# Performance work log

Measured on AMD Instinct MI355X. Metric: run time of the kernel, lower is better.

The kernel has to match this reference:

```python
import jax, jax.numpy as jnp
import numpy as np

N, E, DIN, DOUT, NNZ = 8192, 4096, 256, 128, 65536
TEMP = float(DOUT) ** 0.5
NEG = -1e9


def setup_inputs() -> dict:
    key = jax.random.key(0)
    ks = jax.random.split(key, 8)
    stdv = 1.0 / np.sqrt(DOUT)
    u = lambda k, shp: jax.random.uniform(k, shp, jnp.float32, -stdv, stdv)
    x = jax.random.normal(ks[0], (N, DIN), jnp.float32)
    nodes = jax.random.randint(ks[1], (NNZ,), 0, N, jnp.int32)
    edges = jax.random.randint(ks[2], (NNZ,), 0, E, jnp.int32)
    hyperedge_index = jnp.stack([nodes, edges])  # [2, nnz]
    return {
        "x": x,
        "weight": u(ks[3], (DIN, DOUT)),   # transfer weight
        "weight2": u(ks[4], (DIN, DOUT)),
        "weight3": u(ks[5], (DOUT, DOUT)),
        "bias": u(ks[6], (DOUT,)),
        "q_ctx": u(ks[7], (DOUT,)),        # word_context.weight[0]
        "hyperedge_index": hyperedge_index,
        "num_nodes": N,
        "num_edges": E,
    }


def reference(x, weight, weight2, weight3, bias, q_ctx, hyperedge_index, num_nodes, num_edges):
    # dense incidence H[node, edge] = 1  (hyperedge_preprocess)
    H = jnp.zeros((num_nodes, num_edges), x.dtype).at[
        hyperedge_index[0], hyperedge_index[1]].set(1.0)
    adj = H.T                       # [E, N]  (mask / original attention for attn1)

    x4 = x @ weight2                # [N, D]  x_4att
    xt = x @ weight + bias          # [N, D]  transferred features (v of attn1)

    # ---- attention1: query = shared word-context vector, keys = x4 ----
    row = (q_ctx / TEMP) @ x4.T                    # [N] (q1 rows are identical)
    scores1 = jnp.where(adj == 0, NEG, row[None, :])  # [E, N]
    att1 = jax.nn.softmax(adj, axis=-1) + jax.nn.softmax(scores1, axis=-1)
    edge = att1 @ xt                               # [E, D]

    att2he = att1.T                                # [N, E]

    # ---- attention2: queries = x4, keys = edge @ W3 ----
    edge4 = edge @ weight3                         # [E, D]
    scores2 = jnp.where(adj.T == 0, NEG, (x4 / TEMP) @ edge4.T)  # [N, E]
    att2hn = jax.nn.softmax(adj.T, axis=-1) + jax.nn.softmax(scores2, axis=-1)

    # ---- fused outer-product attention and output projection ----
    A = att2he @ att2he.T + att2hn @ att2hn.T      # [N, N]
    h_prime_g = jax.nn.elu(A @ x4)                 # [N, D]
    return h_prime_g
```

## Files before the change

kernel.cpp:

```cpp
#include <hip/hip_runtime.h>
#include <math.h>

constexpr int Nn   = 8192;
constexpr int Ee   = 4096;
constexpr int DIN  = 256;
constexpr int DOUT = 128;
constexpr int NNZ  = 65536;
constexpr int EC   = 96;
constexpr int NC   = 48;

#define TEMPR 0.08838834764831845f
#define EM1   1.7182818284590452f

typedef __attribute__((ext_vector_type(8))) short short8;
typedef __attribute__((ext_vector_type(4))) float f32x4;

static __device__ __forceinline__ float wave_sum64(float v) {
#pragma unroll
    for (int m = 32; m; m >>= 1) v += __shfl_xor(v, m, 64);
    return v;
}
static __device__ __forceinline__ float wave_max64(float v) {
#pragma unroll
    for (int m = 32; m; m >>= 1) v = fmaxf(v, __shfl_xor(v, m, 64));
    return v;
}
static __device__ __forceinline__ short f2bf(float f) {
    union { float f; unsigned u; } v; v.f = f;
    const unsigned r = (v.u + 0x7FFFu + ((v.u >> 16) & 1u)) >> 16;
    return (short)r;
}
static __device__ __forceinline__ unsigned packbf2(float a, float b) {
    return ((unsigned)(unsigned short)f2bf(a)) |
           (((unsigned)(unsigned short)f2bf(b)) << 16);
}
static __device__ __forceinline__ float2 unpackbf2(unsigned u) {
    union { unsigned u; float f; } lo, hi;
    lo.u = u << 16; hi.u = u & 0xFFFF0000u;
    return make_float2(lo.f, hi.f);
}

__global__ __launch_bounds__(256) void k_ww3(
    const float* __restrict__ W, const float* __restrict__ W2,
    const float* __restrict__ W3, const float* __restrict__ bias,
    short* __restrict__ W2T, short* __restrict__ WWT, float* __restrict__ bW3)
{
    const int b = blockIdx.x;
    const int t = threadIdx.x;
    if (b < 32) {
        __shared__ float sW[8][128];
        const int r0 = b * 8;
        for (int i = t; i < 1024; i += 256)
            sW[i >> 7][i & 127] = W[(size_t)(r0 + (i >> 7)) * DOUT + (i & 127)];
        __syncthreads();
        const int c  = t & 127;
        const int rh = (t >> 7) * 4;
        float acc[4] = {0.f, 0.f, 0.f, 0.f};
        for (int k = 0; k < 128; ++k) {
            const float w3 = W3[(size_t)k * DOUT + c];
#pragma unroll
            for (int i = 0; i < 4; ++i) acc[i] = fmaf(sW[rh + i][k], w3, acc[i]);
        }
#pragma unroll
        for (int i = 0; i < 4; ++i)
            WWT[(size_t)c * DIN + (r0 + rh + i)] = f2bf(acc[i]);
    } else if (b < 40) {
        const int k0 = (b - 32) * 32;
        for (int i = t; i < 32 * 128; i += 256) {
            const int k = k0 + (i >> 7);
            const int n = i & 127;
            W2T[(size_t)n * DIN + k] = f2bf(W2[(size_t)k * DOUT + n]);
        }
    } else {
        if (t < 128) {
            float acc = 0.f;
            for (int k = 0; k < 128; ++k)
                acc = fmaf(bias[k], W3[(size_t)k * DOUT + t], acc);
            bW3[t] = acc;
        }
    }
}

__global__ __launch_bounds__(256) void k_gemm1f(
    const float* __restrict__ x, const short* __restrict__ W2T,
    const short* __restrict__ WWT, const float* __restrict__ bW3,
    const float* __restrict__ q, const int* __restrict__ hidx,
    unsigned* __restrict__ bitmap, int* __restrict__ degE, int* __restrict__ degN,
    int* __restrict__ csrEn, int* __restrict__ csrNe, int* __restrict__ csrNs,
    short* __restrict__ x4b, short* __restrict__ xwb,
    float* __restrict__ rowv, float* __restrict__ csx4, float* __restrict__ csxw)
{
    __shared__ float s4[DOUT], sw[DOUT], srow[16];
    const int t    = threadIdx.x;
    const int lane = t & 63;
    const int wv   = t >> 6;
    const int n16  = lane & 15;
    const int quad = lane >> 4;
    const int r0   = blockIdx.x * 16;
    const int n0   = wv * 32;

    const unsigned gid = blockIdx.x * 256 + t;
    if (gid < NNZ) {
        const int n = hidx[gid];
        const int e = hidx[NNZ + gid];
        const unsigned word = (unsigned)n * (unsigned)Ee + (unsigned)e;
        const unsigned bit  = 1u << (word & 31u);
        const unsigned old  = atomicOr(&bitmap[word >> 5], bit);
        if (!(old & bit)) {
            const int pe = atomicAdd(&degE[e], 1);
            if (pe < EC) {
                csrEn[e * EC + pe] = n;
                const int pn = atomicAdd(&degN[n], 1);
                if (pn < NC) {
                    csrNe[n * NC + pn] = e;
                    csrNs[n * NC + pn] = e * EC + pe;
                }
            }
        }
    }

    f32x4 acc4[2], accw[2];
#pragma unroll
    for (int nt = 0; nt < 2; ++nt) {
        acc4[nt] = (f32x4){0.f, 0.f, 0.f, 0.f};
        accw[nt] = (f32x4){0.f, 0.f, 0.f, 0.f};
    }
#pragma unroll
    for (int k0 = 0; k0 < DIN; k0 += 32) {
        const int kb = k0 + quad * 8;
        const float4 xa = *(const float4*)&x[(size_t)(r0 + n16) * DIN + kb];
        const float4 xb = *(const float4*)&x[(size_t)(r0 + n16) * DIN + kb + 4];
        short8 af;
        af[0] = f2bf(xa.x); af[1] = f2bf(xa.y); af[2] = f2bf(xa.z); af[3] = f2bf(xa.w);
        af[4] = f2bf(xb.x); af[5] = f2bf(xb.y); af[6] = f2bf(xb.z); af[7] = f2bf(xb.w);
#pragma unroll
        for (int nt = 0; nt < 2; ++nt) {
            const int col = n0 + nt * 16 + n16;
            const short8 b4 = *(const short8*)&W2T[(size_t)col * DIN + kb];
            const short8 bw = *(const short8*)&WWT[(size_t)col * DIN + kb];
            acc4[nt] = __builtin_amdgcn_mfma_f32_16x16x32_bf16(af, b4, acc4[nt], 0, 0, 0);
            accw[nt] = __builtin_amdgcn_mfma_f32_16x16x32_bf16(af, bw, accw[nt], 0, 0, 0);
        }
    }

    float bwv[2], qv[2];
#pragma unroll
    for (int nt = 0; nt < 2; ++nt) {
        const int col = n0 + nt * 16 + n16;
        bwv[nt] = bW3[col];
        qv[nt]  = q[col];
    }
#pragma unroll
    for (int nt = 0; nt < 2; ++nt) {
        const int col = n0 + nt * 16 + n16;
#pragma unroll
        for (int reg = 0; reg < 4; ++reg) {
            const int row = r0 + quad * 4 + reg;
            x4b[(size_t)row * DOUT + col] = f2bf(acc4[nt][reg]);
            xwb[(size_t)row * DOUT + col] = f2bf(accw[nt][reg] + bwv[nt]);
        }
    }
    float pr[4];
#pragma unroll
    for (int reg = 0; reg < 4; ++reg)
        pr[reg] = qv[0] * acc4[0][reg] + qv[1] * acc4[1][reg];
#pragma unroll
    for (int m = 8; m; m >>= 1) {
#pragma unroll
        for (int reg = 0; reg < 4; ++reg) pr[reg] += __shfl_xor(pr[reg], m, 64);
    }
    if (t < 16) srow[t] = 0.f;
    if (t < DOUT) { s4[t] = 0.f; sw[t] = 0.f; }
    __syncthreads();
    if (n16 == 0) {
#pragma unroll
        for (int reg = 0; reg < 4; ++reg) atomicAdd(&srow[quad * 4 + reg], pr[reg]);
    }
#pragma unroll
    for (int nt = 0; nt < 2; ++nt) {
        const int col = n0 + nt * 16 + n16;
        const float c4s = acc4[nt][0] + acc4[nt][1] + acc4[nt][2] + acc4[nt][3];
        const float cws = accw[nt][0] + accw[nt][1] + accw[nt][2] + accw[nt][3]
                        + 4.f * bwv[nt];
        atomicAdd(&s4[col], c4s);
        atomicAdd(&sw[col], cws);
    }
    __syncthreads();
    if (t < 16) rowv[r0 + t] = srow[t] * TEMPR;
    if (t < DOUT) { atomicAdd(&csx4[t], s4[t]); atomicAdd(&csxw[t], sw[t]); }
}

__global__ __launch_bounds__(256) void k_edge1(
    const int* __restrict__ degE, const int* __restrict__ csrEn,
    const float* __restrict__ rowv,
    const float* __restrict__ csx4, const float* __restrict__ csxw,
    const unsigned* __restrict__ x4b, const unsigned* __restrict__ xwb,
    float* __restrict__ Sval, unsigned* __restrict__ e4b, unsigned* __restrict__ G1b,
    float* __restrict__ wsArr, float* __restrict__ c2g)
{
    __shared__ int   sN[4][EC];
    __shared__ float sS[4][EC];
    __shared__ float sC2[4];
    const int t    = threadIdx.x;
    const int w    = t >> 6;
    const int lane = t & 63;
    const int e    = blockIdx.x * 4 + w;
    const int deg  = min(degE[e], EC);
    const float ue = deg ? 1.0f / ((float)Nn + (float)deg * EM1) : 2.0f / (float)Nn;

    int   n0 = 0, n1 = 0;
    float r0 = -INFINITY, r1 = -INFINITY;
    if (lane < deg)      { n0 = csrEn[e * EC + lane];      r0 = rowv[n0]; }
    if (lane + 64 < deg) { n1 = csrEn[e * EC + lane + 64]; r1 = rowv[n1]; }
    const float m  = wave_max64(fmaxf(r0, r1));
    const float e0 = (lane < deg)      ? expf(r0 - m) : 0.f;
    const float e1 = (lane + 64 < deg) ? expf(r1 - m) : 0.f;
    const float Z  = wave_sum64(e0 + e1);
    const float inv = deg ? 1.0f / Z : 0.f;
    const float base = EM1 * ue;
    if (lane < deg) {
        const float sv = fmaf(e0, inv, base);
        sN[w][lane] = n0; sS[w][lane] = sv;
        Sval[e * EC + lane] = sv;
        atomicAdd(&wsArr[n0], ue * sv);
    }
    if (lane + 64 < deg) {
        const float sv = fmaf(e1, inv, base);
        sN[w][lane + 64] = n1; sS[w][lane + 64] = sv;
        Sval[e * EC + lane + 64] = sv;
        atomicAdd(&wsArr[n1], ue * sv);
    }

    const float2 cw = *(const float2*)&csxw[lane * 2];
    const float2 c4 = *(const float2*)&csx4[lane * 2];
    float2 aE = make_float2(ue * cw.x, ue * cw.y);
    float2 aG = make_float2(ue * c4.x, ue * c4.y);
    int j = 0;
    for (; j + 8 <= deg; j += 8) {
        int ai[8]; float bi[8]; unsigned tu[8], fu[8];
#pragma unroll
        for (int k = 0; k < 8; ++k) { ai[k] = sN[w][j+k]; bi[k] = sS[w][j+k]; }
#pragma unroll
        for (int k = 0; k < 8; ++k) {
            tu[k] = xwb[(size_t)ai[k] * 64 + lane];
            fu[k] = x4b[(size_t)ai[k] * 64 + lane];
        }
#pragma unroll
        for (int k = 0; k < 8; ++k) {
            const float2 tv = unpackbf2(tu[k]);
            const float2 fv = unpackbf2(fu[k]);
            aE.x = fmaf(bi[k], tv.x, aE.x); aE.y = fmaf(bi[k], tv.y, aE.y);
            aG.x = fmaf(bi[k], fv.x, aG.x); aG.y = fmaf(bi[k], fv.y, aG.y);
        }
    }
    for (; j < deg; ++j) {
        const int   a = sN[w][j];
        const float b = sS[w][j];
        const float2 tv = unpackbf2(xwb[(size_t)a * 64 + lane]);
        const float2 fv = unpackbf2(x4b[(size_t)a * 64 + lane]);
        aE.x = fmaf(b, tv.x, aE.x); aE.y = fmaf(b, tv.y, aE.y);
        aG.x = fmaf(b, fv.x, aG.x); aG.y = fmaf(b, fv.y, aG.y);
    }
    e4b[(size_t)e * 64 + lane] = packbf2(aE.x, aE.y);
    G1b[(size_t)e * 64 + lane] = packbf2(aG.x, aG.y);

    if (lane == 0) sC2[w] = ue * ue;
    __syncthreads();
    if (t == 0) atomicAdd(c2g, sC2[0] + sC2[1] + sC2[2] + sC2[3]);
}

__global__ __launch_bounds__(256) void k_node2(
    const int* __restrict__ degN, const int* __restrict__ csrNe,
    const int* __restrict__ csrNs, const unsigned* __restrict__ x4b,
    const unsigned* __restrict__ e4b, const float* __restrict__ wsArr,
    float* __restrict__ Tval, float* __restrict__ vArr,
    float* __restrict__ vxg, float* __restrict__ twxg, float* __restrict__ wsxg)
{
    __shared__ float sx[4][DOUT];
    __shared__ float sVX[DOUT], sTX[DOUT], sWX[DOUT];
    const int t    = threadIdx.x;
    const int w    = t >> 6;
    const int lane = t & 63;

    float2 vxa = {0,0}, twa = {0,0}, wsa = {0,0};
#pragma unroll
    for (int s = 0; s < 2; ++s) {
        const int n   = blockIdx.x * 8 + w * 2 + s;
        const int deg = min(degN[n], NC);
        const float vn = deg ? 1.0f / ((float)Ee + (float)deg * EM1) : 2.0f / (float)Ee;
        const float2 xv = unpackbf2(x4b[(size_t)n * 64 + lane]);
        __syncthreads();
        sx[w][lane * 2 + 0] = xv.x;
        sx[w][lane * 2 + 1] = xv.y;
        __syncthreads();
        int ej = 0, slot = 0;
        if (lane < deg) { ej = csrNe[n * NC + lane]; slot = csrNs[n * NC + lane]; }
        const uint4* er = (const uint4*)&e4b[(size_t)ej * 64];
        float dot = 0.f;
#pragma unroll
        for (int c0 = 0; c0 < 16; c0 += 8) {
            uint4 ev[8];
#pragma unroll
            for (int k = 0; k < 8; ++k) ev[k] = er[c0 + k];
#pragma unroll
            for (int k = 0; k < 8; ++k) {
                const int base = (c0 + k) * 8;
                const float2 e0 = unpackbf2(ev[k].x);
                const float2 e1 = unpackbf2(ev[k].y);
                const float2 e2 = unpackbf2(ev[k].z);
                const float2 e3 = unpackbf2(ev[k].w);
                dot = fmaf(e0.x, sx[w][base + 0], dot);
                dot = fmaf(e0.y, sx[w][base + 1], dot);
                dot = fmaf(e1.x, sx[w][base + 2], dot);
                dot = fmaf(e1.y, sx[w][base + 3], dot);
                dot = fmaf(e2.x, sx[w][base + 4], dot);
                dot = fmaf(e2.y, sx[w][base + 5], dot);
                dot = fmaf(e3.x, sx[w][base + 6], dot);
                dot = fmaf(e3.y, sx[w][base + 7], dot);
            }
        }
        const float sj = (lane < deg) ? dot * TEMPR : -INFINITY;
        const float m  = wave_max64(sj);
        const float ex = (lane < deg) ? expf(sj - m) : 0.f;
        const float Z  = wave_sum64(ex);
        if (lane < deg) Tval[slot] = fmaf(EM1, vn, ex / Z);
        if (lane == 0) vArr[n] = vn;
        const float tw  = deg ? fmaf((float)deg * EM1, vn, 1.0f) : 0.f;
        const float wsn = wsArr[n];
        vxa.x = fmaf(vn,  xv.x, vxa.x); vxa.y = fmaf(vn,  xv.y, vxa.y);
        twa.x = fmaf(tw,  xv.x, twa.x); twa.y = fmaf(tw,  xv.y, twa.y);
        wsa.x = fmaf(wsn, xv.x, wsa.x); wsa.y = fmaf(wsn, xv.y, wsa.y);
    }
    __syncthreads();
    if (t < DOUT) { sVX[t] = 0.f; sTX[t] = 0.f; sWX[t] = 0.f; }
    __syncthreads();
    atomicAdd(&sVX[lane*2+0], vxa.x); atomicAdd(&sVX[lane*2+1], vxa.y);
    atomicAdd(&sTX[lane*2+0], twa.x); atomicAdd(&sTX[lane*2+1], twa.y);
    atomicAdd(&sWX[lane*2+0], wsa.x); atomicAdd(&sWX[lane*2+1], wsa.y);
    __syncthreads();
    if (t < DOUT) {
        atomicAdd(&vxg[t],  sVX[t]);
        atomicAdd(&twxg[t], sTX[t]);
        atomicAdd(&wsxg[t], sWX[t]);
    }
}

__global__ __launch_bounds__(256) void k_g2(
    const int* __restrict__ degE, const int* __restrict__ csrEn,
    const float* __restrict__ Tval, const float* __restrict__ vxg,
    const unsigned* __restrict__ x4b, unsigned* __restrict__ G2b)
{
    const int t    = threadIdx.x;
    const int w    = t >> 6;
    const int lane = t & 63;
    const int e    = blockIdx.x * 4 + w;
    const int deg  = min(degE[e], EC);
    float2 acc = *(const float2*)&vxg[lane * 2];
    int j = 0;
    for (; j + 8 <= deg; j += 8) {
        int ai[8]; float bi[8]; unsigned fu[8];
#pragma unroll
        for (int k = 0; k < 8; ++k) { ai[k] = csrEn[e*EC+j+k]; bi[k] = Tval[e*EC+j+k]; }
#pragma unroll
        for (int k = 0; k < 8; ++k)
            fu[k] = x4b[(size_t)ai[k] * 64 + lane];
#pragma unroll
        for (int k = 0; k < 8; ++k) {
            const float2 fv = unpackbf2(fu[k]);
            acc.x = fmaf(bi[k], fv.x, acc.x); acc.y = fmaf(bi[k], fv.y, acc.y);
        }
    }
    for (; j < deg; ++j) {
        const int   a = csrEn[e*EC+j];
        const float b = Tval[e*EC+j];
        const float2 fv = unpackbf2(x4b[(size_t)a * 64 + lane]);
        acc.x = fmaf(b, fv.x, acc.x); acc.y = fmaf(b, fv.y, acc.y);
    }
    G2b[(size_t)e * 64 + lane] = packbf2(acc.x, acc.y);
}

__global__ __launch_bounds__(256) void k_final(
    const int* __restrict__ degN, const int* __restrict__ csrNe,
    const int* __restrict__ csrNs, const float* __restrict__ Sval,
    const float* __restrict__ Tval, const float* __restrict__ vArr,
    const float* __restrict__ c2g, const float* __restrict__ csx4,
    const float* __restrict__ wsxg, const float* __restrict__ vxg,
    const float* __restrict__ twxg,
    const unsigned* __restrict__ G1b, const unsigned* __restrict__ G2b,
    float* __restrict__ out)
{
    const int t    = threadIdx.x;
    const int w    = t >> 6;
    const int lane = t & 63;
    const int n    = blockIdx.x * 4 + w;
    const int deg  = min(degN[n], NC);
    const float vn = vArr[n];
    const float c2 = *c2g;
    const float2 c4v = *(const float2*)&csx4[lane * 2];
    const float2 wsv = *(const float2*)&wsxg[lane * 2];
    const float2 vxv = *(const float2*)&vxg[lane * 2];
    const float2 twv = *(const float2*)&twxg[lane * 2];
    float2 acc;
    acc.x = fmaf(c2, c4v.x, wsv.x) + vn * fmaf((float)Ee, vxv.x, twv.x);
    acc.y = fmaf(c2, c4v.y, wsv.y) + vn * fmaf((float)Ee, vxv.y, twv.y);
    int j = 0;
    for (; j + 4 <= deg; j += 4) {
        int ei[4], si[4]; float sv[4], tv[4]; unsigned g1u[4], g2u[4];
#pragma unroll
        for (int k = 0; k < 4; ++k) {
            ei[k] = csrNe[n*NC+j+k]; si[k] = csrNs[n*NC+j+k];
        }
#pragma unroll
        for (int k = 0; k < 4; ++k) {
            sv[k] = Sval[si[k]]; tv[k] = Tval[si[k]];
            g1u[k] = G1b[(size_t)ei[k] * 64 + lane];
            g2u[k] = G2b[(size_t)ei[k] * 64 + lane];
        }
#pragma unroll
        for (int k = 0; k < 4; ++k) {
            const float2 g1 = unpackbf2(g1u[k]);
            const float2 g2 = unpackbf2(g2u[k]);
            acc.x = fmaf(sv[k], g1.x, acc.x); acc.y = fmaf(sv[k], g1.y, acc.y);
            acc.x = fmaf(tv[k], g2.x, acc.x); acc.y = fmaf(tv[k], g2.y, acc.y);
        }
    }
    for (; j < deg; ++j) {
        const int ea = csrNe[n*NC+j];
        const int sa = csrNs[n*NC+j];
        const float sva = Sval[sa], tva = Tval[sa];
        const float2 g1a = unpackbf2(G1b[(size_t)ea * 64 + lane]);
        const float2 g2a = unpackbf2(G2b[(size_t)ea * 64 + lane]);
        acc.x = fmaf(sva, g1a.x, acc.x); acc.y = fmaf(sva, g1a.y, acc.y);
        acc.x = fmaf(tva, g2a.x, acc.x); acc.y = fmaf(tva, g2a.y, acc.y);
    }
    acc.x = acc.x > 0.f ? acc.x : expm1f(acc.x);
    acc.y = acc.y > 0.f ? acc.y : expm1f(acc.y);
    *(float2*)&out[(size_t)n * DOUT + lane * 2] = acc;
}

extern "C" void kernel_launch(void* const* d_in, const int* in_sizes, int n_in,
                              void* d_out, int out_size, void* d_ws, size_t ws_size,
                              hipStream_t stream)
{
    const float* x    = (const float*)d_in[0];
    const float* W    = (const float*)d_in[1];
    const float* W2   = (const float*)d_in[2];
    const float* W3   = (const float*)d_in[3];
    const float* bias = (const float*)d_in[4];
    const float* q    = (const float*)d_in[5];
    const int*   hidx = (const int*)d_in[6];
    float* out = (float*)d_out;

    char* wsp = (char*)d_ws;
    size_t o = 0;
    auto take = [&](size_t bytes) {
        size_t r = o; o += (bytes + 255) & ~(size_t)255; return r;
    };
    unsigned* bitmap = (unsigned*)(wsp + take((size_t)Nn * Ee / 8));
    int*   degE  = (int*)  (wsp + take((size_t)Ee * 4));
    int*   degN  = (int*)  (wsp + take((size_t)Nn * 4));
    float* wsArr = (float*)(wsp + take((size_t)Nn * 4));
    float* c2g   = (float*)(wsp + take(4));
    float* csx4  = (float*)(wsp + take(DOUT * 4));
    float* csxw  = (float*)(wsp + take(DOUT * 4));
    float* vxg   = (float*)(wsp + take(DOUT * 4));
    float* twxg  = (float*)(wsp + take(DOUT * 4));
    float* wsxg  = (float*)(wsp + take(DOUT * 4));
    const size_t zbytes = o;
    short* x4b   = (short*)(wsp + take((size_t)Nn * DOUT * 2));
    short* xwb   = (short*)(wsp + take((size_t)Nn * DOUT * 2));
    float* rowv  = (float*)(wsp + take((size_t)Nn * 4));
    float* vArr  = (float*)(wsp + take((size_t)Nn * 4));
    int*   csrEn = (int*)  (wsp + take((size_t)Ee * EC * 4));
    float* Sval  = (float*)(wsp + take((size_t)Ee * EC * 4));
    float* Tval  = (float*)(wsp + take((size_t)Ee * EC * 4));
    int*   csrNe = (int*)  (wsp + take((size_t)Nn * NC * 4));
    int*   csrNs = (int*)  (wsp + take((size_t)Nn * NC * 4));
    unsigned* e4b = (unsigned*)(wsp + take((size_t)Ee * DOUT * 2));
    unsigned* G1b = (unsigned*)(wsp + take((size_t)Ee * DOUT * 2));
    unsigned* G2b = (unsigned*)(wsp + take((size_t)Ee * DOUT * 2));
    short* W2T   = (short*)(wsp + take((size_t)DOUT * DIN * 2));
    short* WWT   = (short*)(wsp + take((size_t)DOUT * DIN * 2));
    float* bW3   = (float*)(wsp + take(DOUT * 4));
    (void)ws_size; (void)in_sizes; (void)n_in; (void)out_size;

    hipMemsetAsync(d_ws, 0, zbytes, stream);

    k_ww3   <<<41,      256, 0, stream>>>(W, W2, W3, bias, W2T, WWT, bW3);
    k_gemm1f<<<Nn / 16, 256, 0, stream>>>(x, W2T, WWT, bW3, q, hidx,
                                          bitmap, degE, degN, csrEn, csrNe, csrNs,
                                          x4b, xwb, rowv, csx4, csxw);
    k_edge1 <<<Ee / 4,  256, 0, stream>>>(degE, csrEn, rowv, csx4, csxw,
                                          (const unsigned*)x4b, (const unsigned*)xwb,
                                          Sval, e4b, G1b, wsArr, c2g);
    k_node2 <<<Nn / 8,  256, 0, stream>>>(degN, csrNe, csrNs,
                                          (const unsigned*)x4b, e4b, wsArr,
                                          Tval, vArr, vxg, twxg, wsxg);
    k_g2    <<<Ee / 4,  256, 0, stream>>>(degE, csrEn, Tval, vxg,
                                          (const unsigned*)x4b, G2b);
    k_final <<<Nn / 4,  256, 0, stream>>>(degN, csrNe, csrNs, Sval, Tval, vArr,
                                          c2g, csx4, wsxg, vxg, twxg, G1b, G2b, out);
}
```

Baseline: 185.4 us.

## Fuse all stages into one cooperative megakernel with grid-wide syncs

Replaces the workspace memset and six separate kernel launches with a single cooperative kernel of 256 blocks of 1024 threads. The stages are separated by grid.sync(), and the weight preprocessing and workspace zeroing are folded into the first phase. The aim is to remove launch gaps and per-kernel tail effects between short dependent stages. In exchange it adds five grid barriers and fixes occupancy at one large block per CU. The old multi-kernel path is kept as a fallback if the cooperative launch fails.

```diff
diff --git a/kernel.cpp b/kernel.cpp
--- a/kernel.cpp
+++ b/kernel.cpp
@@ -1,5 +1,8 @@
 #include <hip/hip_runtime.h>
+#include <hip/hip_cooperative_groups.h>
 #include <math.h>
+
+namespace cg = cooperative_groups;
 
 constexpr int Nn   = 8192;
 constexpr int Ee   = 4096;
@@ -8,6 +11,9 @@
 constexpr int NNZ  = 65536;
 constexpr int EC   = 96;
 constexpr int NC   = 48;
+constexpr int CBLK = 256;
+constexpr int CTHR = 1024;
+constexpr int CWAV = CBLK * CTHR / 64;
 
 #define TEMPR 0.08838834764831845f
 #define EM1   1.7182818284590452f
@@ -38,6 +44,380 @@
     union { unsigned u; float f; } lo, hi;
     lo.u = u << 16; hi.u = u & 0xFFFF0000u;
     return make_float2(lo.f, hi.f);
+}
+
+struct Prm {
+    const float* x; const float* W; const float* W2; const float* W3;
+    const float* bias; const float* q; const int* hidx;
+    void* zbase; unsigned zTotal16;
+    unsigned* bitmap; int* degE; int* degN;
+    float* wsArr; float* c2g;
+    float* csx4; float* csxw; float* vxg; float* twxg; float* wsxg;
+    short* x4b; short* xwb; float* rowv; float* vArr;
+    int* csrEn; float* Sval; float* Tval; int* csrNe; int* csrNs;
+    unsigned* e4b; unsigned* G1b; unsigned* G2b;
+    short* W2T; short* WWT; float* bW3;
+    float* out;
+};
+
+union SMem {
+    struct {
+        float s4[DOUT]; float sw[DOUT]; float srow[2][16];
+    } g;
+    struct {
+        int sN[16][EC]; float sS[16][EC]; float c2s[16];
+    } e;
+    struct {
+        float sx[16][DOUT];
+        float a[DOUT]; float b[DOUT]; float c[DOUT];
+    } r;
+};
+
+__global__ __launch_bounds__(CTHR) void mega2(Prm p)
+{
+    __shared__ SMem sm;
+    cg::grid_group grid = cg::this_grid();
+
+    const int t    = threadIdx.x;
+    const int lane = t & 63;
+    const int w    = t >> 6;
+    const unsigned gid = blockIdx.x * CTHR + t;
+    const int u    = blockIdx.x * 16 + w;
+    const int n16  = lane & 15;
+    const int quad = lane >> 4;
+
+    if (gid < 8192) {
+        const int b  = gid >> 8;
+        const int tt = gid & 255;
+        const int c  = tt & 127;
+        const int rh = (tt >> 7) * 4;
+        const int r0 = b * 8;
+        float acc[4] = {0.f, 0.f, 0.f, 0.f};
+        for (int k = 0; k < 128; ++k) {
+            const float w3 = p.W3[(size_t)k * DOUT + c];
+#pragma unroll
+            for (int i = 0; i < 4; ++i)
+                acc[i] = fmaf(p.W[(size_t)(r0 + rh + i) * DOUT + k], w3, acc[i]);
+        }
+#pragma unroll
+        for (int i = 0; i < 4; ++i)
+            p.WWT[(size_t)c * DIN + (r0 + rh + i)] = f2bf(acc[i]);
+    } else if (gid < 10240) {
+        const int idx = gid - 8192;
+        const int k0  = (idx >> 8) * 32;
+        const int tt  = idx & 255;
+        for (int i = tt; i < 32 * 128; i += 256) {
+            const int k = k0 + (i >> 7);
+            const int n = i & 127;
+            p.W2T[(size_t)n * DIN + k] = f2bf(p.W2[(size_t)k * DOUT + n]);
+        }
+    } else if (gid < 10368) {
+        const int c = gid - 10240;
+        float acc = 0.f;
+        for (int k = 0; k < 128; ++k)
+            acc = fmaf(p.bias[k], p.W3[(size_t)k * DOUT + c], acc);
+        p.bW3[c] = acc;
+    } else {
+        uint4 z; z.x = z.y = z.z = z.w = 0u;
+        uint4* zp = (uint4*)p.zbase;
+        for (unsigned i = gid - 10368; i < p.zTotal16; i += CBLK * CTHR - 10368)
+            zp[i] = z;
+    }
+    grid.sync();
+
+    if (gid < NNZ) {
+        const int n = p.hidx[gid];
+        const int e = p.hidx[NNZ + gid];
+        const unsigned word = (unsigned)n * (unsigned)Ee + (unsigned)e;
+        const unsigned bit  = 1u << (word & 31u);
+        const unsigned old  = atomicOr(&p.bitmap[word >> 5], bit);
+        if (!(old & bit)) {
+            const int pe = atomicAdd(&p.degE[e], 1);
+            if (pe < EC) {
+                p.csrEn[e * EC + pe] = n;
+                const int pn = atomicAdd(&p.degN[n], 1);
+                if (pn < NC) {
+                    p.csrNe[n * NC + pn] = e;
+                    p.csrNs[n * NC + pn] = e * EC + pe;
+                }
+            }
+        }
+    }
+    {
+        const int tile = u >> 3;
+        const int r0   = tile * 16;
+        const int col0 = (u & 7) * 16;
+        const int col  = col0 + n16;
+        f32x4 acc4 = (f32x4){0.f, 0.f, 0.f, 0.f};
+        f32x4 accw = (f32x4){0.f, 0.f, 0.f, 0.f};
+#pragma unroll
+        for (int k0 = 0; k0 < DIN; k0 += 32) {
+            const int kb = k0 + quad * 8;
+            const float4 xa = *(const float4*)&p.x[(size_t)(r0 + n16) * DIN + kb];
+            const float4 xb = *(const float4*)&p.x[(size_t)(r0 + n16) * DIN + kb + 4];
+            short8 af;
+            af[0] = f2bf(xa.x); af[1] = f2bf(xa.y); af[2] = f2bf(xa.z); af[3] = f2bf(xa.w);
+            af[4] = f2bf(xb.x); af[5] = f2bf(xb.y); af[6] = f2bf(xb.z); af[7] = f2bf(xb.w);
+            const short8 b4 = *(const short8*)&p.W2T[(size_t)col * DIN + kb];
+            const short8 bw = *(const short8*)&p.WWT[(size_t)col * DIN + kb];
+            acc4 = __builtin_amdgcn_mfma_f32_16x16x32_bf16(af, b4, acc4, 0, 0, 0);
+            accw = __builtin_amdgcn_mfma_f32_16x16x32_bf16(af, bw, accw, 0, 0, 0);
+        }
+        const float bwv = p.bW3[col];
+        const float qv  = p.q[col];
+#pragma unroll
+        for (int reg = 0; reg < 4; ++reg) {
+            const int row = r0 + quad * 4 + reg;
+            p.x4b[(size_t)row * DOUT + col] = f2bf(acc4[reg]);
+            p.xwb[(size_t)row * DOUT + col] = f2bf(accw[reg] + bwv);
+        }
+        float pr[4];
+#pragma unroll
+        for (int reg = 0; reg < 4; ++reg) pr[reg] = qv * acc4[reg];
+#pragma unroll
+        for (int m = 8; m; m >>= 1) {
+#pragma unroll
+            for (int reg = 0; reg < 4; ++reg) pr[reg] += __shfl_xor(pr[reg], m, 64);
+        }
+        if (t < 32) sm.g.srow[t >> 4][t & 15] = 0.f;
+        if (t < DOUT) { sm.g.s4[t] = 0.f; sm.g.sw[t] = 0.f; }
+        __syncthreads();
+        const int team = w >> 3;
+        if (n16 == 0) {
+#pragma unroll
+            for (int reg = 0; reg < 4; ++reg)
+                atomicAdd(&sm.g.srow[team][quad * 4 + reg], pr[reg]);
+        }
+        const float c4s = acc4[0] + acc4[1] + acc4[2] + acc4[3];
+        const float cws = accw[0] + accw[1] + accw[2] + accw[3] + 4.f * bwv;
+        atomicAdd(&sm.g.s4[col], c4s);
+        atomicAdd(&sm.g.sw[col], cws);
+        __syncthreads();
+        if (t < 32)
+            p.rowv[(blockIdx.x * 2 + (t >> 4)) * 16 + (t & 15)] =
+                sm.g.srow[t >> 4][t & 15] * TEMPR;
+        if (t < DOUT) {
+            atomicAdd(&p.csx4[t], sm.g.s4[t]);
+            atomicAdd(&p.csxw[t], sm.g.sw[t]);
+        }
+    }
+    grid.sync();
+
+    {
+        const int e   = u;
+        const int deg = min(p.degE[e], EC);
+        const float ue = deg ? 1.0f / ((float)Nn + (float)deg * EM1) : 2.0f / (float)Nn;
+        int   n0 = 0, n1 = 0;
+        float r0 = -INFINITY, r1 = -INFINITY;
+        if (lane < deg)      { n0 = p.csrEn[e * EC + lane];      r0 = p.rowv[n0]; }
+        if (lane + 64 < deg) { n1 = p.csrEn[e * EC + lane + 64]; r1 = p.rowv[n1]; }
+        const float m  = wave_max64(fmaxf(r0, r1));
+        const float e0 = (lane < deg)      ? expf(r0 - m) : 0.f;
+        const float e1 = (lane + 64 < deg) ? expf(r1 - m) : 0.f;
+        const float Z  = wave_sum64(e0 + e1);
+        const float inv = deg ? 1.0f / Z : 0.f;
+        const float base = EM1 * ue;
+        if (lane < deg) {
+            const float sv = fmaf(e0, inv, base);
+            sm.e.sN[w][lane] = n0; sm.e.sS[w][lane] = sv;
+            p.Sval[e * EC + lane] = sv;
+            atomicAdd(&p.wsArr[n0], ue * sv);
+        }
+        if (lane + 64 < deg) {
+            const float sv = fmaf(e1, inv, base);
+            sm.e.sN[w][lane + 64] = n1; sm.e.sS[w][lane + 64] = sv;
+            p.Sval[e * EC + lane + 64] = sv;
+            atomicAdd(&p.wsArr[n1], ue * sv);
+        }
+        const float2 cw = *(const float2*)&p.csxw[lane * 2];
+        const float2 c4 = *(const float2*)&p.csx4[lane * 2];
+        float2 aE = make_float2(ue * cw.x, ue * cw.y);
+        float2 aG = make_float2(ue * c4.x, ue * c4.y);
+        const unsigned* x4u = (const unsigned*)p.x4b;
+        const unsigned* xwu = (const unsigned*)p.xwb;
+        int j = 0;
+        for (; j + 8 <= deg; j += 8) {
+            int ai[8]; float bi[8]; unsigned tu[8], fu[8];
+#pragma unroll
+            for (int k = 0; k < 8; ++k) { ai[k] = sm.e.sN[w][j+k]; bi[k] = sm.e.sS[w][j+k]; }
+#pragma unroll
+            for (int k = 0; k < 8; ++k) {
+                tu[k] = xwu[(size_t)ai[k] * 64 + lane];
+                fu[k] = x4u[(size_t)ai[k] * 64 + lane];
+            }
+#pragma unroll
+            for (int k = 0; k < 8; ++k) {
+                const float2 tv = unpackbf2(tu[k]);
+                const float2 fv = unpackbf2(fu[k]);
+                aE.x = fmaf(bi[k], tv.x, aE.x); aE.y = fmaf(bi[k], tv.y, aE.y);
+                aG.x = fmaf(bi[k], fv.x, aG.x); aG.y = fmaf(bi[k], fv.y, aG.y);
+            }
+        }
+        for (; j < deg; ++j) {
+            const int   a = sm.e.sN[w][j];
+            const float b = sm.e.sS[w][j];
+            const float2 tv = unpackbf2(xwu[(size_t)a * 64 + lane]);
+            const float2 fv = unpackbf2(x4u[(size_t)a * 64 + lane]);
+            aE.x = fmaf(b, tv.x, aE.x); aE.y = fmaf(b, tv.y, aE.y);
+            aG.x = fmaf(b, fv.x, aG.x); aG.y = fmaf(b, fv.y, aG.y);
+        }
+        p.e4b[(size_t)e * 64 + lane] = packbf2(aE.x, aE.y);
+        p.G1b[(size_t)e * 64 + lane] = packbf2(aG.x, aG.y);
+        if (lane == 0) sm.e.c2s[w] = ue * ue;
+        __syncthreads();
+        if (t == 0) {
+            float s = 0.f;
+#pragma unroll
+            for (int k = 0; k < 16; ++k) s += sm.e.c2s[k];
+            atomicAdd(p.c2g, s);
+        }
+    }
+    grid.sync();
+
+    {
+        float2 vxa = {0,0}, twa = {0,0}, wsa = {0,0};
+        const unsigned* x4u = (const unsigned*)p.x4b;
+#pragma unroll
+        for (int s = 0; s < 2; ++s) {
+            const int n   = u + s * CWAV;
+            const int deg = min(p.degN[n], NC);
+            const float vn = deg ? 1.0f / ((float)Ee + (float)deg * EM1) : 2.0f / (float)Ee;
+            const float2 xv = unpackbf2(x4u[(size_t)n * 64 + lane]);
+            sm.r.sx[w][lane * 2 + 0] = xv.x;
+            sm.r.sx[w][lane * 2 + 1] = xv.y;
+            __builtin_amdgcn_s_waitcnt(0);
+            int ej = 0, slot = 0;
+            if (lane < deg) { ej = p.csrNe[n * NC + lane]; slot = p.csrNs[n * NC + lane]; }
+            const uint4* er = (const uint4*)&p.e4b[(size_t)ej * 64];
+            float dot = 0.f;
+#pragma unroll
+            for (int c0 = 0; c0 < 16; c0 += 8) {
+                uint4 ev[8];
+#pragma unroll
+                for (int k = 0; k < 8; ++k) ev[k] = er[c0 + k];
+#pragma unroll
+                for (int k = 0; k < 8; ++k) {
+                    const int base = (c0 + k) * 8;
+                    const float2 e0 = unpackbf2(ev[k].x);
+                    const float2 e1 = unpackbf2(ev[k].y);
+                    const float2 e2 = unpackbf2(ev[k].z);
+                    const float2 e3 = unpackbf2(ev[k].w);
+                    dot = fmaf(e0.x, sm.r.sx[w][base + 0], dot);
+                    dot = fmaf(e0.y, sm.r.sx[w][base + 1], dot);
+                    dot = fmaf(e1.x, sm.r.sx[w][base + 2], dot);
+                    dot = fmaf(e1.y, sm.r.sx[w][base + 3], dot);
+                    dot = fmaf(e2.x, sm.r.sx[w][base + 4], dot);
+                    dot = fmaf(e2.y, sm.r.sx[w][base + 5], dot);
+                    dot = fmaf(e3.x, sm.r.sx[w][base + 6], dot);
+                    dot = fmaf(e3.y, sm.r.sx[w][base + 7], dot);
+                }
+            }
+            const float sj = (lane < deg) ? dot * TEMPR : -INFINITY;
+            const float m  = wave_max64(sj);
+            const float ex = (lane < deg) ? expf(sj - m) : 0.f;
+            const float Z  = wave_sum64(ex);
+            if (lane < deg) p.Tval[slot] = fmaf(EM1, vn, ex / Z);
+            if (lane == 0) p.vArr[n] = vn;
+            const float tw  = deg ? fmaf((float)deg * EM1, vn, 1.0f) : 0.f;
+            const float wsn = p.wsArr[n];
+            vxa.x = fmaf(vn,  xv.x, vxa.x); vxa.y = fmaf(vn,  xv.y, vxa.y);
+            twa.x = fmaf(tw,  xv.x, twa.x); twa.y = fmaf(tw,  xv.y, twa.y);
+            wsa.x = fmaf(wsn, xv.x, wsa.x); wsa.y = fmaf(wsn, xv.y, wsa.y);
+        }
+        __syncthreads();
+        if (t < DOUT) { sm.r.a[t] = 0.f; sm.r.b[t] = 0.f; sm.r.c[t] = 0.f; }
+        __syncthreads();
+        atomicAdd(&sm.r.a[lane*2+0], vxa.x); atomicAdd(&sm.r.a[lane*2+1], vxa.y);
+        atomicAdd(&sm.r.b[lane*2+0], twa.x); atomicAdd(&sm.r.b[lane*2+1], twa.y);
+        atomicAdd(&sm.r.c[lane*2+0], wsa.x); atomicAdd(&sm.r.c[lane*2+1], wsa.y);
+        __syncthreads();
+        if (t < DOUT) {
+            atomicAdd(&p.vxg[t],  sm.r.a[t]);
+            atomicAdd(&p.twxg[t], sm.r.b[t]);
+            atomicAdd(&p.wsxg[t], sm.r.c[t]);
+        }
+    }
+    grid.sync();
+
+    {
+        const int e   = u;
+        const int deg = min(p.degE[e], EC);
+        const unsigned* x4u = (const unsigned*)p.x4b;
+        float2 acc = *(const float2*)&p.vxg[lane * 2];
+        int j = 0;
+        for (; j + 8 <= deg; j += 8) {
+            int ai[8]; float bi[8]; unsigned fu[8];
+#pragma unroll
+            for (int k = 0; k < 8; ++k) {
+                ai[k] = p.csrEn[e*EC+j+k]; bi[k] = p.Tval[e*EC+j+k];
+            }
+#pragma unroll
+            for (int k = 0; k < 8; ++k) fu[k] = x4u[(size_t)ai[k] * 64 + lane];
+#pragma unroll
+            for (int k = 0; k < 8; ++k) {
+                const float2 fv = unpackbf2(fu[k]);
+                acc.x = fmaf(bi[k], fv.x, acc.x); acc.y = fmaf(bi[k], fv.y, acc.y);
+            }
+        }
+        for (; j < deg; ++j) {
+            const int   a = p.csrEn[e*EC+j];
+            const float b = p.Tval[e*EC+j];
+            const float2 fv = unpackbf2(x4u[(size_t)a * 64 + lane]);
+            acc.x = fmaf(b, fv.x, acc.x); acc.y = fmaf(b, fv.y, acc.y);
+        }
+        p.G2b[(size_t)e * 64 + lane] = packbf2(acc.x, acc.y);
+    }
+    grid.sync();
+
+    {
+        const float c2 = *p.c2g;
+        const float2 c4v = *(const float2*)&p.csx4[lane * 2];
+        const float2 wsv = *(const float2*)&p.wsxg[lane * 2];
+        const float2 vxv = *(const float2*)&p.vxg[lane * 2];
+        const float2 twv = *(const float2*)&p.twxg[lane * 2];
+#pragma unroll
+        for (int s = 0; s < 2; ++s) {
+            const int n   = u + s * CWAV;
+            const int deg = min(p.degN[n], NC);
+            const float vn = p.vArr[n];
+            float2 acc;
+            acc.x = fmaf(c2, c4v.x, wsv.x) + vn * fmaf((float)Ee, vxv.x, twv.x);
+            acc.y = fmaf(c2, c4v.y, wsv.y) + vn * fmaf((float)Ee, vxv.y, twv.y);
+            int j = 0;
+            for (; j + 4 <= deg; j += 4) {
+                int ei[4], si[4]; float sv[4], tv[4]; unsigned g1u[4], g2u[4];
+#pragma unroll
+                for (int k = 0; k < 4; ++k) {
+                    ei[k] = p.csrNe[n*NC+j+k]; si[k] = p.csrNs[n*NC+j+k];
+                }
+#pragma unroll
+                for (int k = 0; k < 4; ++k) {
+                    sv[k] = p.Sval[si[k]]; tv[k] = p.Tval[si[k]];
+                    g1u[k] = p.G1b[(size_t)ei[k] * 64 + lane];
+                    g2u[k] = p.G2b[(size_t)ei[k] * 64 + lane];
+                }
+#pragma unroll
+                for (int k = 0; k < 4; ++k) {
+                    const float2 g1 = unpackbf2(g1u[k]);
+                    const float2 g2 = unpackbf2(g2u[k]);
+                    acc.x = fmaf(sv[k], g1.x, acc.x); acc.y = fmaf(sv[k], g1.y, acc.y);
+                    acc.x = fmaf(tv[k], g2.x, acc.x); acc.y = fmaf(tv[k], g2.y, acc.y);
+                }
+            }
+            for (; j < deg; ++j) {
+                const int ea = p.csrNe[n*NC+j];
+                const int sa = p.csrNs[n*NC+j];
+                const float sva = p.Sval[sa], tva = p.Tval[sa];
+                const float2 g1a = unpackbf2(p.G1b[(size_t)ea * 64 + lane]);
+                const float2 g2a = unpackbf2(p.G2b[(size_t)ea * 64 + lane]);
+                acc.x = fmaf(sva, g1a.x, acc.x); acc.y = fmaf(sva, g1a.y, acc.y);
+                acc.x = fmaf(tva, g2a.x, acc.x); acc.y = fmaf(tva, g2a.y, acc.y);
+            }
+            acc.x = acc.x > 0.f ? acc.x : expm1f(acc.x);
+            acc.y = acc.y > 0.f ? acc.y : expm1f(acc.y);
+            *(float2*)&p.out[(size_t)n * DOUT + lane * 2] = acc;
+        }
+    }
 }
 
 __global__ __launch_bounds__(256) void k_ww3(
@@ -142,7 +522,6 @@
             accw[nt] = __builtin_amdgcn_mfma_f32_16x16x32_bf16(af, bw, accw[nt], 0, 0, 0);
         }
     }
-
     float bwv[2], qv[2];
 #pragma unroll
     for (int nt = 0; nt < 2; ++nt) {
@@ -230,7 +609,6 @@
         Sval[e * EC + lane + 64] = sv;
         atomicAdd(&wsArr[n1], ue * sv);
     }
-
     const float2 cw = *(const float2*)&csxw[lane * 2];
     const float2 c4 = *(const float2*)&csx4[lane * 2];
     float2 aE = make_float2(ue * cw.x, ue * cw.y);
@@ -442,62 +820,78 @@
                               void* d_out, int out_size, void* d_ws, size_t ws_size,
                               hipStream_t stream)
 {
-    const float* x    = (const float*)d_in[0];
-    const float* W    = (const float*)d_in[1];
-    const float* W2   = (const float*)d_in[2];
-    const float* W3   = (const float*)d_in[3];
-    const float* bias = (const float*)d_in[4];
-    const float* q    = (const float*)d_in[5];
-    const int*   hidx = (const int*)d_in[6];
-    float* out = (float*)d_out;
+    Prm prm;
+    prm.x    = (const float*)d_in[0];
+    prm.W    = (const float*)d_in[1];
+    prm.W2   = (const float*)d_in[2];
+    prm.W3   = (const float*)d_in[3];
+    prm.bias = (const float*)d_in[4];
+    prm.q    = (const float*)d_in[5];
+    prm.hidx = (const int*)d_in[6];
+    prm.out  = (float*)d_out;
 
     char* wsp = (char*)d_ws;
     size_t o = 0;
     auto take = [&](size_t bytes) {
         size_t r = o; o += (bytes + 255) & ~(size_t)255; return r;
     };
-    unsigned* bitmap = (unsigned*)(wsp + take((size_t)Nn * Ee / 8));
-    int*   degE  = (int*)  (wsp + take((size_t)Ee * 4));
-    int*   degN  = (int*)  (wsp + take((size_t)Nn * 4));
-    float* wsArr = (float*)(wsp + take((size_t)Nn * 4));
-    float* c2g   = (float*)(wsp + take(4));
-    float* csx4  = (float*)(wsp + take(DOUT * 4));
-    float* csxw  = (float*)(wsp + take(DOUT * 4));
-    float* vxg   = (float*)(wsp + take(DOUT * 4));
-    float* twxg  = (float*)(wsp + take(DOUT * 4));
-    float* wsxg  = (float*)(wsp + take(DOUT * 4));
+    prm.bitmap = (unsigned*)(wsp + take((size_t)Nn * Ee / 8));
+    prm.degE   = (int*)  (wsp + take((size_t)Ee * 4));
+    prm.degN   = (int*)  (wsp + take((size_t)Nn * 4));
+    prm.wsArr  = (float*)(wsp + take((size_t)Nn * 4));
+    prm.c2g    = (float*)(wsp + take(4));
+    prm.csx4   = (float*)(wsp + take(DOUT * 4));
+    prm.csxw   = (float*)(wsp + take(DOUT * 4));
+    prm.vxg    = (float*)(wsp + take(DOUT * 4));
+    prm.twxg   = (float*)(wsp + take(DOUT * 4));
+    prm.wsxg   = (float*)(wsp + take(DOUT * 4));
+    prm.zbase  = d_ws;
     const size_t zbytes = o;
-    short* x4b   = (short*)(wsp + take((size_t)Nn * DOUT * 2));
-    short* xwb   = (short*)(wsp + take((size_t)Nn * DOUT * 2));
-    float* rowv  = (float*)(wsp + take((size_t)Nn * 4));
-    float* vArr  = (float*)(wsp + take((size_t)Nn * 4));
-    int*   csrEn = (int*)  (wsp + take((size_t)Ee * EC * 4));
-    float* Sval  = (float*)(wsp + take((size_t)Ee * EC * 4));
-    float* Tval  = (float*)(wsp + take((size_t)Ee * EC * 4));
-    int*   csrNe = (int*)  (wsp + take((size_t)Nn * NC * 4));
-    int*   csrNs = (int*)  (wsp + take((size_t)Nn * NC * 4));
-    unsigned* e4b = (unsigned*)(wsp + take((size_t)Ee * DOUT * 2));
-    unsigned* G1b = (unsigned*)(wsp + take((size_t)Ee * DOUT * 2));
-    unsigned* G2b = (unsigned*)(wsp + take((size_t)Ee * DOUT * 2));
-    short* W2T   = (short*)(wsp + take((size_t)DOUT * DIN * 2));
-    short* WWT   = (short*)(wsp + take((size_t)DOUT * DIN * 2));
-    float* bW3   = (float*)(wsp + take(DOUT * 4));
+    prm.zTotal16 = (unsigned)(zbytes / 16);
+    prm.x4b   = (short*)(wsp + take((size_t)Nn * DOUT * 2));
+    prm.xwb   = (short*)(wsp + take((size_t)Nn * DOUT * 2));
+    prm.rowv  = (float*)(wsp + take((size_t)Nn * 4));
+    prm.vArr  = (float*)(wsp + take((size_t)Nn * 4));
+    prm.csrEn = (int*)  (wsp + take((size_t)Ee * EC * 4));
+    prm.Sval  = (float*)(wsp + take((size_t)Ee * EC * 4));
+    prm.Tval  = (float*)(wsp + take((size_t)Ee * EC * 4));
+    prm.csrNe = (int*)  (wsp + take((size_t)Nn * NC * 4));
+    prm.csrNs = (int*)  (wsp + take((size_t)Nn * NC * 4));
+    prm.e4b   = (unsigned*)(wsp + take((size_t)Ee * DOUT * 2));
+    prm.G1b   = (unsigned*)(wsp + take((size_t)Ee * DOUT * 2));
+    prm.G2b   = (unsigned*)(wsp + take((size_t)Ee * DOUT * 2));
+    prm.W2T   = (short*)(wsp + take((size_t)DOUT * DIN * 2));
+    prm.WWT   = (short*)(wsp + take((size_t)DOUT * DIN * 2));
+    prm.bW3   = (float*)(wsp + take(DOUT * 4));
     (void)ws_size; (void)in_sizes; (void)n_in; (void)out_size;
 
-    hipMemsetAsync(d_ws, 0, zbytes, stream);
-
-    k_ww3   <<<41,      256, 0, stream>>>(W, W2, W3, bias, W2T, WWT, bW3);
-    k_gemm1f<<<Nn / 16, 256, 0, stream>>>(x, W2T, WWT, bW3, q, hidx,
-                                          bitmap, degE, degN, csrEn, csrNe, csrNs,
-                                          x4b, xwb, rowv, csx4, csxw);
-    k_edge1 <<<Ee / 4,  256, 0, stream>>>(degE, csrEn, rowv, csx4, csxw,
-                                          (const unsigned*)x4b, (const unsigned*)xwb,
-                                          Sval, e4b, G1b, wsArr, c2g);
-    k_node2 <<<Nn / 8,  256, 0, stream>>>(degN, csrNe, csrNs,
-                                          (const unsigned*)x4b, e4b, wsArr,
-                                          Tval, vArr, vxg, twxg, wsxg);
-    k_g2    <<<Ee / 4,  256, 0, stream>>>(degE, csrEn, Tval, vxg,
-                                          (const unsigned*)x4b, G2b);
-    k_final <<<Nn / 4,  256, 0, stream>>>(degN, csrNe, csrNs, Sval, Tval, vArr,
-                                          c2g, csx4, wsxg, vxg, twxg, G1b, G2b, out);
-}
+    void* args[] = { &prm };
+    hipError_t err = hipLaunchCooperativeKernel((void*)mega2, dim3(CBLK),
+                                                dim3(CTHR), args, 0, stream);
+    if (err != hipSuccess) {
+        hipMemsetAsync(d_ws, 0, zbytes, stream);
+        k_ww3   <<<41,      256, 0, stream>>>(prm.x ? prm.W : prm.W, prm.W2, prm.W3,
+                                              prm.bias, prm.W2T, prm.WWT, prm.bW3);
+        k_gemm1f<<<Nn / 16, 256, 0, stream>>>(prm.x, prm.W2T, prm.WWT, prm.bW3,
+                                              prm.q, prm.hidx, prm.bitmap, prm.degE,
+                                              prm.degN, prm.csrEn, prm.csrNe, prm.csrNs,
+                                              prm.x4b, prm.xwb, prm.rowv,
+                                              prm.csx4, prm.csxw);
+        k_edge1 <<<Ee / 4,  256, 0, stream>>>(prm.degE, prm.csrEn, prm.rowv,
+                                              prm.csx4, prm.csxw,
+                                              (const unsigned*)prm.x4b,
+                                              (const unsigned*)prm.xwb,
+                                              prm.Sval, prm.e4b, prm.G1b,
+                                              prm.wsArr, prm.c2g);
+        k_node2 <<<Nn / 8,  256, 0, stream>>>(prm.degN, prm.csrNe, prm.csrNs,
+                                              (const unsigned*)prm.x4b, prm.e4b,
+                                              prm.wsArr, prm.Tval, prm.vArr,
+                                              prm.vxg, prm.twxg, prm.wsxg);
+        k_g2    <<<Ee / 4,  256, 0, stream>>>(prm.degE, prm.csrEn, prm.Tval, prm.vxg,
+                                              (const unsigned*)prm.x4b, prm.G2b);
+        k_final <<<Nn / 4,  256, 0, stream>>>(prm.degN, prm.csrNe, prm.csrNs,
+                                              prm.Sval, prm.Tval, prm.vArr,
+                                              prm.c2g, prm.csx4, prm.wsxg, prm.vxg,
+                                              prm.twxg, prm.G1b, prm.G2b, prm.out);
+    }
+}
```

Result: slower. 320.9 us (+73.1%).
